# Optimization experiments

Hardware: AMD Instinct MI355X
Metric: run time of the kernel (lower is better)

## Reference

```python
import jax, jax.numpy as jnp
import numpy as np

IN_F, OUT_F, M, BATCH = 64, 64, 20, 1024


def setup_inputs() -> dict:
    key = jax.random.key(0)
    k1, k2 = jax.random.split(key)
    x = jax.random.normal(k1, (BATCH, IN_F), dtype=jnp.float32)
    # parameters, initialized as in the torch module
    z = jnp.tile(jnp.linspace(-1.5, 1.5, M, dtype=jnp.float32).reshape(1, 1, M), (OUT_F, IN_F, 1))
    q_mu = jax.random.normal(k2, (OUT_F, IN_F, M), dtype=jnp.float32) * 0.05
    q_log_var = jnp.full((OUT_F, IN_F, M), -3.0, dtype=jnp.float32)
    log_scale = jnp.zeros((OUT_F, IN_F), dtype=jnp.float32)
    log_variance = jnp.full((OUT_F, IN_F), -1.0, dtype=jnp.float32)
    return {"x": x, "z": z, "q_mu": q_mu, "q_log_var": q_log_var,
            "log_scale": log_scale, "log_variance": log_variance}


def reference(x, z, q_mu, q_log_var, log_scale, log_variance):
    """SVGP-KAN layer, RBF kernel, deterministic input path (x_var = 1e-6).

    Per edge (o,i): basis-function GP f(x) = sum_m w_m k(x, z_m),
    w_m ~ N(q_mu, q_var), k(x,z) = sig2 * exp(-(x-z)^2 / (2 l^2)).
    Gaussian input x ~ N(mu, v) -> closed-form moments (Psi statistics).
    """
    x_mean = x
    x_var = jnp.full_like(x, 1e-6)

    q_var = jnp.clip(jnp.exp(q_log_var), 1e-5)          # [O,I,M]
    sig2 = jnp.clip(jnp.exp(log_variance), 1e-5)        # [O,I]
    ell = jnp.clip(jnp.exp(log_scale), 0.1)             # [O,I] (rbf min_scale=0.1)

    # broadcast: batch x out x in x inducing
    xm = x_mean[:, None, :, None]                       # [B,1,I,1]
    xv = x_var[:, None, :, None]                        # [B,1,I,1]
    zz = z[None]                                        # [1,O,I,M]
    l2 = (ell * ell)[None, :, :, None]                  # [1,O,I,1]
    s2 = sig2[None, :, :, None]                         # [1,O,I,1]

    d2 = (xm - zz) ** 2                                 # [B,O,I,M]
    den1 = l2 + xv
    psi1 = s2 * jnp.sqrt(l2 / den1) * jnp.exp(-d2 / (2.0 * den1))  # E[k(x,z_m)]
    den2 = l2 + 2.0 * xv
    ek2 = (s2 * s2) * jnp.sqrt(l2 / den2) * jnp.exp(-d2 / den2)     # E[k(x,z_m)^2]

    qm = q_mu[None]                                     # [1,O,I,M]
    qv = q_var[None]
    edge_mean = jnp.sum(psi1 * qm, axis=-1)             # [B,O,I]
    edge_var = jnp.sum(ek2 * (qm * qm + qv) - psi1 * psi1 * (qm * qm), axis=-1)
    edge_var = jnp.clip(edge_var, 0.0)                  # [B,O,I]

    y_mean = edge_mean.sum(axis=2)                      # [B,O]
    y_var = edge_var.sum(axis=2)                        # [B,O]
    return y_mean, y_var
```

## Files before the change

### kernel.cpp

```cpp
#include <hip/hip_runtime.h>
#include <hip/hip_bf16.h>

#define OUT_F 64
#define IN_F 64
#define M_PTS 20
#define BATCH 1024

#if __has_builtin(__builtin_amdgcn_exp2f)
#define EXP2(x) __builtin_amdgcn_exp2f(x)
#else
#define EXP2(x) exp2f(x)
#endif

__device__ float2 g_c2[OUT_F * M_PTS * IN_F];
__device__ float4 g_aux[OUT_F * IN_F];

__global__ __launch_bounds__(256) void prep_kernel(
    const float* __restrict__ z, const float* __restrict__ q_mu,
    const float* __restrict__ q_log_var, const float* __restrict__ log_scale,
    const float* __restrict__ log_variance)
{
    int idx = blockIdx.x * 256 + threadIdx.x;
    if (idx >= OUT_F * M_PTS * IN_F) return;
    int i  = idx & 63;
    int om = idx >> 6;
    int m  = om % M_PTS;
    int o  = om / M_PTS;
    int e  = o * IN_F + i;
    int ge = e * M_PTS + m;

    const float LOG2E = 1.4426950408889634f;
    float ell  = fmaxf(expf(log_scale[e]), 0.1f);
    float l2   = ell * ell;
    float sig2 = fmaxf(expf(log_variance[e]), 1e-5f);
    float den1 = l2 + 1e-6f;
    float den2 = l2 + 2e-6f;
    float c1   = sig2 * sqrtf(l2 / den1);
    float c2   = sig2 * sig2 * sqrtf(l2 / den2);
    float s    = sqrtf(0.5f * LOG2E / den1);

    float qm  = q_mu[ge];
    float qv  = fmaxf(expf(q_log_var[ge]), 1e-5f);
    float qmc = c1 * qm;
    float A   = c2 * (qm * qm + qv);

    g_c2[idx] = make_float2(qmc, A - qmc * qmc);
    if (m == 0) {
        float z0  = z[ge];
        float z19 = z[e * M_PTS + (M_PTS - 1)];
        float delta = (z19 - z0) * (1.0f / (M_PTS - 1));
        float sd = s * delta;
        g_aux[e] = make_float4(s, s * z0, 2.0f * sd, -(sd * sd));
    }
}

__global__ __launch_bounds__(256, 6) void gpkan_main(
    const float* __restrict__ x, float* __restrict__ out)
{
    __shared__ float2 red[4][8][66];

    const int tid  = threadIdx.x;
    const int lane = tid & 63;
    const int wv   = __builtin_amdgcn_readfirstlane(tid >> 6);
    const int o    = blockIdx.y * 4 + wv;
    const int bc   = blockIdx.x;

    float4 aux = g_aux[(o << 6) + lane];
    const float s = aux.x, sz0 = aux.y, cu1 = aux.z, cu0 = aux.w;
    const float v = EXP2(cu0 + cu0);

    float2 c2[M_PTS];
    #pragma unroll
    for (int m = 0; m < M_PTS; ++m)
        c2[m] = g_c2[((o * M_PTS + m) << 6) + lane];

    #pragma unroll
    for (int b8 = 0; b8 < 8; ++b8) {
        const int b = (bc << 3) + b8;
        float xb = x[(b << 6) + lane];
        float dx = fmaf(s, xb, -sz0);
        float t  = EXP2(-(dx * dx));
        float ua = fminf(fmaf(cu1, dx, cu0), 60.0f);
        float w  = EXP2(ua);

        float em = 0.0f, ev = 0.0f;
        #pragma unroll
        for (int m = 0; m < M_PTS; ++m) {
            em = fmaf(c2[m].x, t, em);
            ev = fmaf(c2[m].y, t * t, ev);
            if (m < M_PTS - 1) { t *= w; w *= v; }
        }
        red[wv][b8][lane] = make_float2(em, fmaxf(ev, 0.0f));
    }
    __syncthreads();

    const int seg = lane >> 3, b8r = lane & 7;
    const float4* rp = reinterpret_cast<const float4*>(&red[wv][b8r][seg << 3]);
    float sm = 0.0f, sv = 0.0f;
    #pragma unroll
    for (int j = 0; j < 4; ++j) {
        float4 p = rp[j];
        sm += p.x + p.z;
        sv += p.y + p.w;
    }
    sm += __shfl_xor(sm, 8);  sv += __shfl_xor(sv, 8);
    sm += __shfl_xor(sm, 16); sv += __shfl_xor(sv, 16);
    sm += __shfl_xor(sm, 32); sv += __shfl_xor(sv, 32);

    if (lane < 8) {
        int b = (bc << 3) + lane;
        out[(b << 6) + o] = sm;
        out[(BATCH << 6) + (b << 6) + o] = sv;
    }
}

extern "C" void kernel_launch(void* const* d_in, const int* in_sizes, int n_in,
                              void* d_out, int out_size, void* d_ws, size_t ws_size,
                              hipStream_t stream) {
    const float* x            = (const float*)d_in[0];
    const float* z            = (const float*)d_in[1];
    const float* q_mu         = (const float*)d_in[2];
    const float* q_log_var    = (const float*)d_in[3];
    const float* log_scale    = (const float*)d_in[4];
    const float* log_variance = (const float*)d_in[5];
    float* out = (float*)d_out;

    prep_kernel<<<(OUT_F * M_PTS * IN_F + 255) / 256, 256, 0, stream>>>(
        z, q_mu, q_log_var, log_scale, log_variance);
    gpkan_main<<<dim3(BATCH / 8, OUT_F / 4), 256, 0, stream>>>(x, out);
}
```

Baseline: 22.54 us.

## Use packed FP32 math, single-wave blocks, and shuffle-only transpose reduction

The inner basis loop is rewritten to use v_pk_mul_f32/v_pk_fma_f32 on even/odd inducing-point pairs, with coefficients re-laid out in prep as pairs. The kernel changes from 256-thread blocks over 4 outputs × 8 rows to 64-thread single-wave blocks handling one output and 4 rows, giving 16384 blocks. Shared-memory reduction and __syncthreads are replaced by a butterfly shuffle transpose-reduce. This cuts ALU instructions and removes LDS sync, at the cost of many more small blocks, less reuse of the coefficient loads per block, and a smaller clamp on the exponent argument.

```diff
diff --git a/kernel.cpp b/kernel.cpp
--- a/kernel.cpp
+++ b/kernel.cpp
@@ -4,6 +4,7 @@
 #define OUT_F 64
 #define IN_F 64
 #define M_PTS 20
+#define NPAIR (M_PTS / 2)
 #define BATCH 1024
 
 #if __has_builtin(__builtin_amdgcn_exp2f)
@@ -11,8 +12,21 @@
 #else
 #define EXP2(x) exp2f(x)
 #endif
+#define LOG2E 1.4426950408889634f
 
-__device__ float2 g_c2[OUT_F * M_PTS * IN_F];
+typedef __attribute__((ext_vector_type(2))) float f32x2;
+
+static __device__ __forceinline__ f32x2 pk_mul(f32x2 a, f32x2 b) {
+    f32x2 d;
+    asm("v_pk_mul_f32 %0, %1, %2" : "=v"(d) : "v"(a), "v"(b));
+    return d;
+}
+static __device__ __forceinline__ void pk_fma_acc(f32x2& acc, f32x2 a, f32x2 b) {
+    asm("v_pk_fma_f32 %0, %1, %2, %0" : "+v"(acc) : "v"(a), "v"(b));
+}
+
+__device__ float g_qmcP[OUT_F * NPAIR * IN_F * 2];
+__device__ float g_BP  [OUT_F * NPAIR * IN_F * 2];
 __device__ float4 g_aux[OUT_F * IN_F];
 
 __global__ __launch_bounds__(256) void prep_kernel(
@@ -29,7 +43,6 @@
     int e  = o * IN_F + i;
     int ge = e * M_PTS + m;
 
-    const float LOG2E = 1.4426950408889634f;
     float ell  = fmaxf(expf(log_scale[e]), 0.1f);
     float l2   = ell * ell;
     float sig2 = fmaxf(expf(log_variance[e]), 1e-5f);
@@ -43,8 +56,11 @@
     float qv  = fmaxf(expf(q_log_var[ge]), 1e-5f);
     float qmc = c1 * qm;
     float A   = c2 * (qm * qm + qv);
+    float B   = A - qmc * qmc;
 
-    g_c2[idx] = make_float2(qmc, A - qmc * qmc);
+    int pidx = (((o * NPAIR + (m >> 1)) << 6) + i) * 2 + (m & 1);
+    g_qmcP[pidx] = qmc;
+    g_BP[pidx]   = B;
     if (m == 0) {
         float z0  = z[ge];
         float z19 = z[e * M_PTS + (M_PTS - 1)];
@@ -54,63 +70,91 @@
     }
 }
 
-__global__ __launch_bounds__(256, 6) void gpkan_main(
+__global__ __launch_bounds__(64, 6) void gpkan_main(
     const float* __restrict__ x, float* __restrict__ out)
 {
-    __shared__ float2 red[4][8][66];
-
-    const int tid  = threadIdx.x;
-    const int lane = tid & 63;
-    const int wv   = __builtin_amdgcn_readfirstlane(tid >> 6);
-    const int o    = blockIdx.y * 4 + wv;
-    const int bc   = blockIdx.x;
+    const int blk  = blockIdx.x;
+    const int o    = blk >> 8;
+    const int bc   = blk & 255;
+    const int lane = threadIdx.x;
 
     float4 aux = g_aux[(o << 6) + lane];
     const float s = aux.x, sz0 = aux.y, cu1 = aux.z, cu0 = aux.w;
-    const float v = EXP2(cu0 + cu0);
+    const float v  = EXP2(cu0 + cu0);
+    const float v2 = v * v;
+    const f32x2 V4 = {v2 * v2, v2 * v2};
 
-    float2 c2[M_PTS];
+    f32x2 qmcP[NPAIR], BP[NPAIR];
     #pragma unroll
-    for (int m = 0; m < M_PTS; ++m)
-        c2[m] = g_c2[((o * M_PTS + m) << 6) + lane];
+    for (int p = 0; p < NPAIR; ++p) {
+        int base = ((o * NPAIR + p) << 6) + lane;
+        qmcP[p] = *reinterpret_cast<const f32x2*>(&g_qmcP[base * 2]);
+        BP[p]   = *reinterpret_cast<const f32x2*>(&g_BP[base * 2]);
+    }
 
+    const float* __restrict__ xg = x + (bc << 8);
+
+    float qa[8];
     #pragma unroll
-    for (int b8 = 0; b8 < 8; ++b8) {
-        const int b = (bc << 3) + b8;
-        float xb = x[(b << 6) + lane];
+    for (int r = 0; r < 4; ++r) {
+        float xb = xg[(r << 6) + lane];
         float dx = fmaf(s, xb, -sz0);
-        float t  = EXP2(-(dx * dx));
-        float ua = fminf(fmaf(cu1, dx, cu0), 60.0f);
-        float w  = EXP2(ua);
+        float t0 = EXP2(-(dx * dx));
+        float ua = fminf(fmaf(cu1, dx, cu0), 30.0f);
+        float w0 = EXP2(ua);
+        float w0sq = w0 * w0;
+        float Mlo  = w0sq * v;
+        f32x2 T = {t0, t0 * w0};
+        f32x2 M = {Mlo, Mlo * v2};
+        f32x2 accE = {0.0f, 0.0f};
+        f32x2 accV = {0.0f, 0.0f};
+        #pragma unroll
+        for (int p = 0; p < NPAIR; ++p) {
+            f32x2 U = pk_mul(T, T);
+            pk_fma_acc(accE, qmcP[p], T);
+            pk_fma_acc(accV, BP[p], U);
+            if (p < NPAIR - 1) {
+                T = pk_mul(T, M);
+                M = pk_mul(M, V4);
+            }
+        }
+        qa[r]     = accE.x + accE.y;
+        qa[4 + r] = fmaxf(accV.x + accV.y, 0.0f);
+    }
 
-        float em = 0.0f, ev = 0.0f;
-        #pragma unroll
-        for (int m = 0; m < M_PTS; ++m) {
-            em = fmaf(c2[m].x, t, em);
-            ev = fmaf(c2[m].y, t * t, ev);
-            if (m < M_PTS - 1) { t *= w; w *= v; }
-        }
-        red[wv][b8][lane] = make_float2(em, fmaxf(ev, 0.0f));
-    }
-    __syncthreads();
+    const bool s5 = (lane & 32) != 0;
+    const bool s4 = (lane & 16) != 0;
+    const bool s3 = (lane & 8) != 0;
 
-    const int seg = lane >> 3, b8r = lane & 7;
-    const float4* rp = reinterpret_cast<const float4*>(&red[wv][b8r][seg << 3]);
-    float sm = 0.0f, sv = 0.0f;
+    float k4[4];
     #pragma unroll
     for (int j = 0; j < 4; ++j) {
-        float4 p = rp[j];
-        sm += p.x + p.z;
-        sv += p.y + p.w;
+        float keep = s5 ? qa[j + 4] : qa[j];
+        float send = s5 ? qa[j] : qa[j + 4];
+        k4[j] = keep + __shfl_xor(send, 32);
     }
-    sm += __shfl_xor(sm, 8);  sv += __shfl_xor(sv, 8);
-    sm += __shfl_xor(sm, 16); sv += __shfl_xor(sv, 16);
-    sm += __shfl_xor(sm, 32); sv += __shfl_xor(sv, 32);
+    float k2[2];
+    #pragma unroll
+    for (int j = 0; j < 2; ++j) {
+        float keep = s4 ? k4[j + 2] : k4[j];
+        float send = s4 ? k4[j] : k4[j + 2];
+        k2[j] = keep + __shfl_xor(send, 16);
+    }
+    float k1;
+    {
+        float keep = s3 ? k2[1] : k2[0];
+        float send = s3 ? k2[0] : k2[1];
+        k1 = keep + __shfl_xor(send, 8);
+    }
+    k1 += __shfl_xor(k1, 4);
+    k1 += __shfl_xor(k1, 2);
+    k1 += __shfl_xor(k1, 1);
 
-    if (lane < 8) {
-        int b = (bc << 3) + lane;
-        out[(b << 6) + o] = sm;
-        out[(BATCH << 6) + (b << 6) + o] = sv;
+    if ((lane & 7) == 0) {
+        int row   = ((lane >> 4) & 1) * 2 + ((lane >> 3) & 1);
+        int is_ev = (lane >> 5) & 1;
+        int b     = (bc << 2) + row;
+        out[is_ev * (BATCH * OUT_F) + b * OUT_F + o] = k1;
     }
 }
 
@@ -127,5 +171,5 @@
 
     prep_kernel<<<(OUT_F * M_PTS * IN_F + 255) / 256, 256, 0, stream>>>(
         z, q_mu, q_log_var, log_scale, log_variance);
-    gpkan_main<<<dim3(BATCH / 8, OUT_F / 4), 256, 0, stream>>>(x, out);
+    gpkan_main<<<256 * OUT_F, 64, 0, stream>>>(x, out);
 }
```

New measurement: 23.68 us. 5.1% more time.
